# Kernel tuning notes

Hardware: AMD Instinct MI355X
Metric: run time of the kernel (lower is better)

Reference implementation:

```python
import jax, jax.numpy as jnp
import numpy as np

E = 1024
H = 8
D = E // H
B = 16384
LN_EPS = 1e-5


def setup_inputs() -> dict:
    key = jax.random.key(0)
    ks = jax.random.split(key, 12)
    s = 1.0 / np.sqrt(E)
    return {
        "image_features": jax.random.normal(ks[0], (B, E), jnp.float32),
        "signal_features": jax.random.normal(ks[1], (B, E), jnp.float32),
        "Wq": jax.random.normal(ks[2], (E, E), jnp.float32) * s,
        "Wk": jax.random.normal(ks[3], (E, E), jnp.float32) * s,
        "Wv": jax.random.normal(ks[4], (E, E), jnp.float32) * s,
        "bq": jnp.zeros((E,), jnp.float32),
        "bk": jnp.zeros((E,), jnp.float32),
        "bv": jnp.zeros((E,), jnp.float32),
        "Wo": jax.random.normal(ks[5], (E, E), jnp.float32) * s,
        "bo": jnp.zeros((E,), jnp.float32),
        "ln_gamma": jnp.ones((E,), jnp.float32),
        "ln_beta": jnp.zeros((E,), jnp.float32),
    }


def _forward(image_features, signal_features, Wq, Wk, Wv, bq, bk, bv, Wo, bo, ln_gamma, ln_beta):
    # query: [B,1,E] from image; key/value: [B,2,E] stacked modalities
    kv = jnp.stack([image_features, signal_features], axis=1)  # [B,2,E]
    # projections (torch Linear convention: x @ W^T + b)
    q = (image_features @ Wq.T + bq).reshape(B, H, 1, D)       # [B,H,1,D]
    k = (kv @ Wk.T + bk).reshape(B, 2, H, D).transpose(0, 2, 1, 3)  # [B,H,2,D]
    v = (kv @ Wv.T + bv).reshape(B, 2, H, D).transpose(0, 2, 1, 3)  # [B,H,2,D]
    scale = 1.0 / jnp.sqrt(jnp.float32(D))
    scores = jnp.einsum("bhqd,bhkd->bhqk", q, k) * scale       # [B,H,1,2]
    attn = jax.nn.softmax(scores, axis=-1)
    ctx = jnp.einsum("bhqk,bhkd->bhqd", attn, v)               # [B,H,1,D]
    ctx = ctx.reshape(B, E)
    attn_out = ctx @ Wo.T + bo
    # residual + LayerNorm (dropout is identity in eval)
    fused = attn_out + image_features
    mu = jnp.mean(fused, axis=-1, keepdims=True)
    var = jnp.var(fused, axis=-1, keepdims=True)
    normed = (fused - mu) * jax.lax.rsqrt(var + LN_EPS)
    return normed * ln_gamma + ln_beta


def reference(image_features, signal_features, Wq, Wk, Wv, bq, bk, bv, Wo, bo, ln_gamma, ln_beta):
    return _forward(image_features, signal_features, Wq, Wk, Wv, bq, bk, bv, Wo, bo, ln_gamma, ln_beta)
```

## Files before the change

### kernel.cpp

```cpp
#include <hip/hip_runtime.h>

#define B_ 16384
#define E_ 1024
#define H_ 8
#define D_ 128
#define BK 32

typedef _Float16 f16;
typedef _Float16 f16x8 __attribute__((ext_vector_type(8)));
typedef float f32x4 __attribute__((ext_vector_type(4)));

__device__ __forceinline__ void gload16(const f16* g, f16* l) {
    __builtin_amdgcn_global_load_lds(
        (const __attribute__((address_space(1))) void*)g,
        (__attribute__((address_space(3))) void*)l, 16, 0, 0);
}


__global__ __launch_bounds__(256) void cvt2_kernel(const float4* __restrict__ s0,
                                                   const float4* __restrict__ s1,
                                                   ushort4* __restrict__ d0,
                                                   ushort4* __restrict__ d1, int n4) {
    const float4* s = blockIdx.y ? s1 : s0;
    ushort4* d = blockIdx.y ? d1 : d0;
    int i = blockIdx.x * 256 + threadIdx.x;
    if (i >= n4) return;
    float4 v = s[i];
    union { ushort4 u; f16 h[4]; } o;
    o.h[0] = (f16)v.x; o.h[1] = (f16)v.y; o.h[2] = (f16)v.z; o.h[3] = (f16)v.w;
    d[i] = o.u;
}

__global__ __launch_bounds__(256) void cvt4_kernel(
    const float4* __restrict__ s0, const float4* __restrict__ s1,
    const float4* __restrict__ s2, const float4* __restrict__ s3,
    ushort4* __restrict__ d0, ushort4* __restrict__ d1,
    ushort4* __restrict__ d2, ushort4* __restrict__ d3, int n4) {
    const float4* s; ushort4* d;
    switch (blockIdx.y) {
        case 0: s = s0; d = d0; break;
        case 1: s = s1; d = d1; break;
        case 2: s = s2; d = d2; break;
        default: s = s3; d = d3; break;
    }
    int i = blockIdx.x * 256 + threadIdx.x;
    if (i >= n4) return;
    float4 v = s[i];
    union { ushort4 u; f16 h[4]; } o;
    o.h[0] = (f16)v.x; o.h[1] = (f16)v.y; o.h[2] = (f16)v.z; o.h[3] = (f16)v.w;
    d[i] = o.u;
}

__global__ __launch_bounds__(256, 2) void qkv_attn_kernel(
    const f16* __restrict__ Xi, const f16* __restrict__ Xs,
    const f16* __restrict__ Wq, const f16* __restrict__ Wk, const f16* __restrict__ Wv,
    const float* __restrict__ bq, const float* __restrict__ bk, const float* __restrict__ bv,
    f16* __restrict__ ctx)
{
    __shared__ f16 sAi[64][BK];
    __shared__ f16 sAs[64][BK];
    __shared__ f16 sWq[128][BK];
    __shared__ f16 sWk[128][BK];
    __shared__ f16 sWv[128][BK];
    __shared__ float sdot[2][64][2];
    __shared__ float sa0[64];

    const int tid  = threadIdx.x;
    const int lane = tid & 63;
    const int wave = tid >> 6;
    const int wr = wave >> 1, wc = wave & 1;
    const int l16 = lane & 15, lq = lane >> 4;

    const int row0 = blockIdx.x * 64;
    const int col0 = blockIdx.y * D_;

    const int lr = lane >> 2;
    const int lc = ((lane & 3) ^ ((lane >> 3) & 3)) * 8;
    const int rc = (lq ^ ((l16 >> 1) & 3)) * 8;

    const f16* gAi = Xi + (size_t)(row0 + wave * 16 + lr) * E_ + lc;
    const f16* gAs = Xs + (size_t)(row0 + wave * 16 + lr) * E_ + lc;
    const size_t woff = (size_t)(col0 + wave * 32 + lr) * E_ + lc;
    const f16* gWq = Wq + woff;
    const f16* gWk = Wk + woff;
    const f16* gWv = Wv + woff;
    const size_t wskip = (size_t)16 * E_;

    f16* lAi  = &sAi[wave * 16][0];
    f16* lAs  = &sAs[wave * 16][0];
    f16* lWq0 = &sWq[wave * 32][0];      f16* lWq1 = &sWq[wave * 32 + 16][0];
    f16* lWk0 = &sWk[wave * 32][0];      f16* lWk1 = &sWk[wave * 32 + 16][0];
    f16* lWv0 = &sWv[wave * 32][0];      f16* lWv1 = &sWv[wave * 32 + 16][0];

    f32x4 zero4 = {0.f, 0.f, 0.f, 0.f};
    f32x4 accQ[2][4], accKi[2][4], accKs[2][4], accVi[2][4], accVs[2][4];
    #pragma unroll
    for (int i = 0; i < 2; i++)
        #pragma unroll
        for (int j = 0; j < 4; j++) {
            accQ[i][j] = zero4; accKi[i][j] = zero4; accKs[i][j] = zero4;
            accVi[i][j] = zero4; accVs[i][j] = zero4;
        }

    for (int kk = 0; kk < E_; kk += BK) {
        gload16(gAi + kk, lAi);
        gload16(gAs + kk, lAs);
        gload16(gWq + kk, lWq0);
        gload16(gWq + wskip + kk, lWq1);
        gload16(gWk + kk, lWk0);
        gload16(gWk + wskip + kk, lWk1);
        gload16(gWv + kk, lWv0);
        gload16(gWv + wskip + kk, lWv1);
        __syncthreads();

        f16x8 aI[2], aS[2], bF[4];
        #pragma unroll
        for (int fr = 0; fr < 2; fr++) {
            aI[fr] = *(const f16x8*)&sAi[wr * 32 + fr * 16 + l16][rc];
            aS[fr] = *(const f16x8*)&sAs[wr * 32 + fr * 16 + l16][rc];
        }
        #pragma unroll
        for (int fc = 0; fc < 4; fc++)
            bF[fc] = *(const f16x8*)&sWq[wc * 64 + fc * 16 + l16][rc];
        #pragma unroll
        for (int fr = 0; fr < 2; fr++)
            #pragma unroll
            for (int fc = 0; fc < 4; fc++)
                accQ[fr][fc] = __builtin_amdgcn_mfma_f32_16x16x32_f16(aI[fr], bF[fc], accQ[fr][fc], 0, 0, 0);
        #pragma unroll
        for (int fc = 0; fc < 4; fc++)
            bF[fc] = *(const f16x8*)&sWk[wc * 64 + fc * 16 + l16][rc];
        #pragma unroll
        for (int fr = 0; fr < 2; fr++)
            #pragma unroll
            for (int fc = 0; fc < 4; fc++) {
                accKi[fr][fc] = __builtin_amdgcn_mfma_f32_16x16x32_f16(aI[fr], bF[fc], accKi[fr][fc], 0, 0, 0);
                accKs[fr][fc] = __builtin_amdgcn_mfma_f32_16x16x32_f16(aS[fr], bF[fc], accKs[fr][fc], 0, 0, 0);
            }
        #pragma unroll
        for (int fc = 0; fc < 4; fc++)
            bF[fc] = *(const f16x8*)&sWv[wc * 64 + fc * 16 + l16][rc];
        #pragma unroll
        for (int fr = 0; fr < 2; fr++)
            #pragma unroll
            for (int fc = 0; fc < 4; fc++) {
                accVi[fr][fc] = __builtin_amdgcn_mfma_f32_16x16x32_f16(aI[fr], bF[fc], accVi[fr][fc], 0, 0, 0);
                accVs[fr][fc] = __builtin_amdgcn_mfma_f32_16x16x32_f16(aS[fr], bF[fc], accVs[fr][fc], 0, 0, 0);
            }
        __syncthreads();
    }

    #pragma unroll
    for (int fc = 0; fc < 4; fc++) {
        int col = col0 + wc * 64 + fc * 16 + l16;
        float bqv = bq[col], bkv = bk[col];
        #pragma unroll
        for (int fr = 0; fr < 2; fr++)
            #pragma unroll
            for (int e = 0; e < 4; e++) {
                accQ[fr][fc][e]  += bqv;
                accKi[fr][fc][e] += bkv;
                accKs[fr][fc][e] += bkv;
            }
    }

    #pragma unroll
    for (int fr = 0; fr < 2; fr++)
        #pragma unroll
        for (int e = 0; e < 4; e++) {
            float d0 = 0.f, d1 = 0.f;
            #pragma unroll
            for (int fc = 0; fc < 4; fc++) {
                d0 += accQ[fr][fc][e] * accKi[fr][fc][e];
                d1 += accQ[fr][fc][e] * accKs[fr][fc][e];
            }
            #pragma unroll
            for (int m = 1; m < 16; m <<= 1) {
                d0 += __shfl_xor(d0, m, 64);
                d1 += __shfl_xor(d1, m, 64);
            }
            if (l16 == 0) {
                int row = wr * 32 + fr * 16 + lq * 4 + e;
                sdot[0][row][wc] = d0;
                sdot[1][row][wc] = d1;
            }
        }
    __syncthreads();
    if (tid < 64) {
        const float scale = 0.088388347648318447f;
        float s0 = (sdot[0][tid][0] + sdot[0][tid][1]) * scale;
        float s1 = (sdot[1][tid][0] + sdot[1][tid][1]) * scale;
        sa0[tid] = 1.0f / (1.0f + expf(s1 - s0));
    }
    __syncthreads();

    #pragma unroll
    for (int fc = 0; fc < 4; fc++) {
        int col = col0 + wc * 64 + fc * 16 + l16;
        float bvv = bv[col];
        #pragma unroll
        for (int fr = 0; fr < 2; fr++)
            #pragma unroll
            for (int e = 0; e < 4; e++) {
                int row = wr * 32 + fr * 16 + lq * 4 + e;
                float a0 = sa0[row];
                float v  = a0 * accVi[fr][fc][e] + (1.0f - a0) * accVs[fr][fc][e] + bvv;
                ctx[(size_t)(row0 + row) * E_ + col] = (f16)v;
            }
    }
}

__global__ __launch_bounds__(256) void out_proj_kernel(
    const f16* __restrict__ A, const f16* __restrict__ Wo, const float* __restrict__ bo,
    const float* __restrict__ resid, float* __restrict__ out)
{
    __shared__ f16 sA[2][128][BK];
    __shared__ f16 sB[2][128][BK];
    const int tid  = threadIdx.x;
    const int lane = tid & 63;
    const int wave = tid >> 6;
    const int wr = wave >> 1, wc = wave & 1;
    const int l16 = lane & 15, lq = lane >> 4;
    const int row0 = blockIdx.x * 128;
    const int col0 = blockIdx.y * 128;

    const int lr = lane >> 2;
    const int lc = ((lane & 3) ^ ((lane >> 3) & 3)) * 8;
    const int rc = (lq ^ ((l16 >> 1) & 3)) * 8;

    const f16* gA0 = A  + (size_t)(row0 + wave * 32 + lr) * E_ + lc;
    const f16* gB0 = Wo + (size_t)(col0 + wave * 32 + lr) * E_ + lc;
    const size_t wskip = (size_t)16 * E_;

    f32x4 zero4 = {0.f, 0.f, 0.f, 0.f};
    f32x4 acc[4][4];
    #pragma unroll
    for (int i = 0; i < 4; i++)
        #pragma unroll
        for (int j = 0; j < 4; j++) acc[i][j] = zero4;

    auto stage = [&](int buf, int kk) {
        gload16(gA0 + kk,         &sA[buf][wave * 32][0]);
        gload16(gA0 + wskip + kk, &sA[buf][wave * 32 + 16][0]);
        gload16(gB0 + kk,         &sB[buf][wave * 32][0]);
        gload16(gB0 + wskip + kk, &sB[buf][wave * 32 + 16][0]);
    };

    stage(0, 0);
    __syncthreads();

    const int NT = E_ / BK;
    for (int t = 0; t < NT; ++t) {
        const int cur = t & 1;
        if (t + 1 < NT) stage(cur ^ 1, (t + 1) * BK);

        f16x8 aF[4], bF[4];
        #pragma unroll
        for (int f = 0; f < 4; f++) {
            aF[f] = *(const f16x8*)&sA[cur][wr * 64 + f * 16 + l16][rc];
            bF[f] = *(const f16x8*)&sB[cur][wc * 64 + f * 16 + l16][rc];
        }
        #pragma unroll
        for (int fr = 0; fr < 4; fr++)
            #pragma unroll
            for (int fc = 0; fc < 4; fc++)
                acc[fr][fc] = __builtin_amdgcn_mfma_f32_16x16x32_f16(aF[fr], bF[fc], acc[fr][fc], 0, 0, 0);
        __syncthreads();
    }

    #pragma unroll
    for (int fc = 0; fc < 4; fc++) {
        int col = col0 + wc * 64 + fc * 16 + l16;
        float bov = bo[col];
        #pragma unroll
        for (int fr = 0; fr < 4; fr++)
            #pragma unroll
            for (int e = 0; e < 4; e++) {
                int row = row0 + wr * 64 + fr * 16 + lq * 4 + e;
                out[(size_t)row * E_ + col] = acc[fr][fc][e] + bov + resid[(size_t)row * E_ + col];
            }
    }
}

__global__ __launch_bounds__(256) void ln_kernel(
    float* __restrict__ x, const float* __restrict__ gamma,
    const float* __restrict__ beta, float* __restrict__ out)
{
    const int row = blockIdx.x;
    const int tid = threadIdx.x;
    const float4* xr = (const float4*)(x + (size_t)row * E_);
    float4 v = xr[tid];
    float s  = v.x + v.y + v.z + v.w;
    float s2 = v.x * v.x + v.y * v.y + v.z * v.z + v.w * v.w;
    #pragma unroll
    for (int m = 1; m < 64; m <<= 1) {
        s  += __shfl_xor(s, m, 64);
        s2 += __shfl_xor(s2, m, 64);
    }
    __shared__ float red[8];
    int wv = tid >> 6, ln = tid & 63;
    if (ln == 0) { red[wv] = s; red[4 + wv] = s2; }
    __syncthreads();
    s  = red[0] + red[1] + red[2] + red[3];
    s2 = red[4] + red[5] + red[6] + red[7];
    float mu  = s * (1.0f / E_);
    float var = s2 * (1.0f / E_) - mu * mu;
    float r   = rsqrtf(var + 1e-5f);
    float4 g  = ((const float4*)gamma)[tid];
    float4 bb = ((const float4*)beta)[tid];
    float4 o;
    o.x = (v.x - mu) * r * g.x + bb.x;
    o.y = (v.y - mu) * r * g.y + bb.y;
    o.z = (v.z - mu) * r * g.z + bb.z;
    o.w = (v.w - mu) * r * g.w + bb.w;
    ((float4*)(out + (size_t)row * E_))[tid] = o;
}

extern "C" void kernel_launch(void* const* d_in, const int* in_sizes, int n_in,
                              void* d_out, int out_size, void* d_ws, size_t ws_size,
                              hipStream_t stream)
{
    (void)in_sizes; (void)n_in; (void)out_size; (void)ws_size;
    const float* image  = (const float*)d_in[0];
    const float* signal = (const float*)d_in[1];
    const float* Wq = (const float*)d_in[2];
    const float* Wk = (const float*)d_in[3];
    const float* Wv = (const float*)d_in[4];
    const float* bq = (const float*)d_in[5];
    const float* bk = (const float*)d_in[6];
    const float* bv = (const float*)d_in[7];
    const float* Wo = (const float*)d_in[8];
    const float* bo = (const float*)d_in[9];
    const float* gamma = (const float*)d_in[10];
    const float* beta  = (const float*)d_in[11];
    float* out = (float*)d_out;

    char* ws = (char*)d_ws;
    f16* Xi16 = (f16*)(ws);
    f16* Xs16 = (f16*)(ws + 32ull * 1024 * 1024);
    f16* Wq16 = (f16*)(ws + 64ull * 1024 * 1024);
    f16* Wk16 = (f16*)(ws + 66ull * 1024 * 1024);
    f16* Wv16 = (f16*)(ws + 68ull * 1024 * 1024);
    f16* Wo16 = (f16*)(ws + 70ull * 1024 * 1024);
    f16* ctx  = (f16*)(ws + 72ull * 1024 * 1024);

    const int nBE4 = B_ * E_ / 4;
    const int nEE4 = E_ * E_ / 4;
    dim3 gX(nBE4 / 256, 2);
    cvt2_kernel<<<gX, 256, 0, stream>>>((const float4*)image, (const float4*)signal,
                                        (ushort4*)Xi16, (ushort4*)Xs16, nBE4);
    dim3 gW(nEE4 / 256, 4);
    cvt4_kernel<<<gW, 256, 0, stream>>>((const float4*)Wq, (const float4*)Wk,
                                        (const float4*)Wv, (const float4*)Wo,
                                        (ushort4*)Wq16, (ushort4*)Wk16,
                                        (ushort4*)Wv16, (ushort4*)Wo16, nEE4);

    dim3 g2(B_ / 64, H_);
    qkv_attn_kernel<<<g2, 256, 0, stream>>>(Xi16, Xs16, Wq16, Wk16, Wv16, bq, bk, bv, ctx);

    dim3 g4(B_ / 128, E_ / 128);
    out_proj_kernel<<<g4, 256, 0, stream>>>(ctx, Wo16, bo, image, out);

    ln_kernel<<<B_, 256, 0, stream>>>(out, gamma, beta, out);
}
```

Measured before the change: 470.3 us.

## Double-buffer QKV LDS tiles and move residual add into LayerNorm with fp16 intermediate

The QKV/attention kernel now double-buffers its LDS tiles so the next K-slice is fetched while the current one is consumed by MFMAs. The output projection writes bias-added results as fp16 into a reused workspace buffer instead of fp32 plus residual. LayerNorm then reads that fp16 buffer and the fp32 residual, adding them before normalisation. This cuts global memory traffic for the intermediate and hides load latency, at the cost of doubled LDS usage and an fp16 rounding of the attention output.

```diff
diff --git a/kernel.cpp b/kernel.cpp
--- a/kernel.cpp
+++ b/kernel.cpp
@@ -57,11 +57,11 @@
     const float* __restrict__ bq, const float* __restrict__ bk, const float* __restrict__ bv,
     f16* __restrict__ ctx)
 {
-    __shared__ f16 sAi[64][BK];
-    __shared__ f16 sAs[64][BK];
-    __shared__ f16 sWq[128][BK];
-    __shared__ f16 sWk[128][BK];
-    __shared__ f16 sWv[128][BK];
+    __shared__ f16 sAi[2][64][BK];
+    __shared__ f16 sAs[2][64][BK];
+    __shared__ f16 sWq[2][128][BK];
+    __shared__ f16 sWk[2][128][BK];
+    __shared__ f16 sWv[2][128][BK];
     __shared__ float sdot[2][64][2];
     __shared__ float sa0[64];
 
@@ -86,12 +86,6 @@
     const f16* gWv = Wv + woff;
     const size_t wskip = (size_t)16 * E_;
 
-    f16* lAi  = &sAi[wave * 16][0];
-    f16* lAs  = &sAs[wave * 16][0];
-    f16* lWq0 = &sWq[wave * 32][0];      f16* lWq1 = &sWq[wave * 32 + 16][0];
-    f16* lWk0 = &sWk[wave * 32][0];      f16* lWk1 = &sWk[wave * 32 + 16][0];
-    f16* lWv0 = &sWv[wave * 32][0];      f16* lWv1 = &sWv[wave * 32 + 16][0];
-
     f32x4 zero4 = {0.f, 0.f, 0.f, 0.f};
     f32x4 accQ[2][4], accKi[2][4], accKs[2][4], accVi[2][4], accVs[2][4];
     #pragma unroll
@@ -102,26 +96,34 @@
             accVi[i][j] = zero4; accVs[i][j] = zero4;
         }
 
-    for (int kk = 0; kk < E_; kk += BK) {
-        gload16(gAi + kk, lAi);
-        gload16(gAs + kk, lAs);
-        gload16(gWq + kk, lWq0);
-        gload16(gWq + wskip + kk, lWq1);
-        gload16(gWk + kk, lWk0);
-        gload16(gWk + wskip + kk, lWk1);
-        gload16(gWv + kk, lWv0);
-        gload16(gWv + wskip + kk, lWv1);
-        __syncthreads();
+    auto stage = [&](int buf, int kk) {
+        gload16(gAi + kk,         &sAi[buf][wave * 16][0]);
+        gload16(gAs + kk,         &sAs[buf][wave * 16][0]);
+        gload16(gWq + kk,         &sWq[buf][wave * 32][0]);
+        gload16(gWq + wskip + kk, &sWq[buf][wave * 32 + 16][0]);
+        gload16(gWk + kk,         &sWk[buf][wave * 32][0]);
+        gload16(gWk + wskip + kk, &sWk[buf][wave * 32 + 16][0]);
+        gload16(gWv + kk,         &sWv[buf][wave * 32][0]);
+        gload16(gWv + wskip + kk, &sWv[buf][wave * 32 + 16][0]);
+    };
+
+    stage(0, 0);
+    __syncthreads();
+
+    const int NT = E_ / BK;
+    for (int t = 0; t < NT; ++t) {
+        const int cur = t & 1;
+        if (t + 1 < NT) stage(cur ^ 1, (t + 1) * BK);
 
         f16x8 aI[2], aS[2], bF[4];
         #pragma unroll
         for (int fr = 0; fr < 2; fr++) {
-            aI[fr] = *(const f16x8*)&sAi[wr * 32 + fr * 16 + l16][rc];
-            aS[fr] = *(const f16x8*)&sAs[wr * 32 + fr * 16 + l16][rc];
+            aI[fr] = *(const f16x8*)&sAi[cur][wr * 32 + fr * 16 + l16][rc];
+            aS[fr] = *(const f16x8*)&sAs[cur][wr * 32 + fr * 16 + l16][rc];
         }
         #pragma unroll
         for (int fc = 0; fc < 4; fc++)
-            bF[fc] = *(const f16x8*)&sWq[wc * 64 + fc * 16 + l16][rc];
+            bF[fc] = *(const f16x8*)&sWq[cur][wc * 64 + fc * 16 + l16][rc];
         #pragma unroll
         for (int fr = 0; fr < 2; fr++)
             #pragma unroll
@@ -129,7 +131,7 @@
                 accQ[fr][fc] = __builtin_amdgcn_mfma_f32_16x16x32_f16(aI[fr], bF[fc], accQ[fr][fc], 0, 0, 0);
         #pragma unroll
         for (int fc = 0; fc < 4; fc++)
-            bF[fc] = *(const f16x8*)&sWk[wc * 64 + fc * 16 + l16][rc];
+            bF[fc] = *(const f16x8*)&sWk[cur][wc * 64 + fc * 16 + l16][rc];
         #pragma unroll
         for (int fr = 0; fr < 2; fr++)
             #pragma unroll
@@ -139,7 +141,7 @@
             }
         #pragma unroll
         for (int fc = 0; fc < 4; fc++)
-            bF[fc] = *(const f16x8*)&sWv[wc * 64 + fc * 16 + l16][rc];
+            bF[fc] = *(const f16x8*)&sWv[cur][wc * 64 + fc * 16 + l16][rc];
         #pragma unroll
         for (int fr = 0; fr < 2; fr++)
             #pragma unroll
@@ -212,7 +214,7 @@
 
 __global__ __launch_bounds__(256) void out_proj_kernel(
     const f16* __restrict__ A, const f16* __restrict__ Wo, const float* __restrict__ bo,
-    const float* __restrict__ resid, float* __restrict__ out)
+    f16* __restrict__ a16)
 {
     __shared__ f16 sA[2][128][BK];
     __shared__ f16 sB[2][128][BK];
@@ -277,19 +279,26 @@
             #pragma unroll
             for (int e = 0; e < 4; e++) {
                 int row = row0 + wr * 64 + fr * 16 + lq * 4 + e;
-                out[(size_t)row * E_ + col] = acc[fr][fc][e] + bov + resid[(size_t)row * E_ + col];
+                a16[(size_t)row * E_ + col] = (f16)(acc[fr][fc][e] + bov);
             }
     }
 }
 
 __global__ __launch_bounds__(256) void ln_kernel(
-    float* __restrict__ x, const float* __restrict__ gamma,
-    const float* __restrict__ beta, float* __restrict__ out)
+    const f16* __restrict__ a16, const float* __restrict__ resid,
+    const float* __restrict__ gamma, const float* __restrict__ beta,
+    float* __restrict__ out)
 {
     const int row = blockIdx.x;
     const int tid = threadIdx.x;
-    const float4* xr = (const float4*)(x + (size_t)row * E_);
-    float4 v = xr[tid];
+    union { ushort4 u; f16 h[4]; } ua;
+    ua.u = ((const ushort4*)(a16 + (size_t)row * E_))[tid];
+    float4 rv = ((const float4*)(resid + (size_t)row * E_))[tid];
+    float4 v;
+    v.x = (float)ua.h[0] + rv.x;
+    v.y = (float)ua.h[1] + rv.y;
+    v.z = (float)ua.h[2] + rv.z;
+    v.w = (float)ua.h[3] + rv.w;
     float s  = v.x + v.y + v.z + v.w;
     float s2 = v.x * v.x + v.y * v.y + v.z * v.z + v.w * v.w;
     #pragma unroll
@@ -343,6 +352,7 @@
     f16* Wv16 = (f16*)(ws + 68ull * 1024 * 1024);
     f16* Wo16 = (f16*)(ws + 70ull * 1024 * 1024);
     f16* ctx  = (f16*)(ws + 72ull * 1024 * 1024);
+    f16* a16  = Xi16;
 
     const int nBE4 = B_ * E_ / 4;
     const int nEE4 = E_ * E_ / 4;
@@ -359,7 +369,7 @@
     qkv_attn_kernel<<<g2, 256, 0, stream>>>(Xi16, Xs16, Wq16, Wk16, Wv16, bq, bk, bv, ctx);
 
     dim3 g4(B_ / 128, E_ / 128);
-    out_proj_kernel<<<g4, 256, 0, stream>>>(ctx, Wo16, bo, image, out);
-
-    ln_kernel<<<B_, 256, 0, stream>>>(out, gamma, beta, out);
-}
+    out_proj_kernel<<<g4, 256, 0, stream>>>(ctx, Wo16, bo, a16);
+
+    ln_kernel<<<B_, 256, 0, stream>>>(a16, image, gamma, beta, out);
+}
```

Result: no change. 476.5 us (+1.3%).
